# Optimization experiments

Measured on AMD Instinct MI355X. Metric: run time of the kernel, lower is better.

The kernel has to match this reference:

```python
import jax, jax.numpy as jnp
import numpy as np

GAMMA = 0.3      # LinearSpike surrogate slope (Bellec et al. 2018)
TIMESTEPS = 8
DROPOUT = 0.2

@jax.custom_vjp
def spike_fn(mem_thr):
    # forward: Heaviside spike; backward: piecewise-linear surrogate
    return (mem_thr > 0).astype(mem_thr.dtype)

def _spike_fwd(m):
    return (m > 0).astype(m.dtype), m

def _spike_bwd(m, g):
    return (GAMMA * jnp.maximum(1.0 - jnp.abs(m), 0.0) * g,)

spike_fn.defvjp(_spike_fwd, _spike_bwd)

def conv(x, w, stride=1, pad=1):
    return jax.lax.conv_general_dilated(
        x, w, (stride, stride), [(pad, pad), (pad, pad)],
        dimension_numbers=('NCHW', 'OIHW', 'NCHW'))

def avgpool2(x):
    B, C, H, W = x.shape
    return x.reshape(B, C, H // 2, 2, W // 2, 2).mean(axis=(3, 5))

def lif(mem, delta, leak, thr):
    mem = leak * mem + delta                  # leaky integrate
    mem_thr = mem / thr - 1.0                 # normalized membrane
    out = spike_fn(mem_thr)                   # binary spike
    mem = mem - thr * (mem_thr > 0).astype(mem.dtype)  # soft reset
    return mem, out

def setup_inputs() -> dict:
    key = jax.random.key(0)
    ks = jax.random.split(key, 24)
    B = 32
    def w(k, o, i, kh):
        std = float(np.sqrt(2.0 / (kh * kh * o)))  # matches _initialize_weights2
        return jax.random.normal(k, (o, i, kh, kh), jnp.float32) * std
    def mask(k, shape):
        keep = jax.random.bernoulli(k, 1.0 - DROPOUT, shape)
        return keep.astype(jnp.float32) / (1.0 - DROPOUT)
    return {
        'x': jax.random.normal(ks[0], (B, 3, 32, 32), jnp.float32),
        'w_pre0': w(ks[1], 64, 3, 3),
        'w_pre1': w(ks[2], 64, 64, 3),
        'w_pre2': w(ks[3], 64, 64, 3),
        'w1a': w(ks[4], 64, 64, 3),  'w1b': w(ks[5], 64, 64, 3),
        'w2a': w(ks[6], 128, 64, 3), 'w2b': w(ks[7], 128, 128, 3), 'w2i': w(ks[8], 128, 64, 1),
        'w3a': w(ks[9], 256, 128, 3), 'w3b': w(ks[10], 256, 256, 3), 'w3i': w(ks[11], 256, 128, 1),
        'w4a': w(ks[12], 512, 256, 3), 'w4b': w(ks[13], 512, 512, 3), 'w4i': w(ks[14], 512, 256, 1),
        'w_fc': jax.random.normal(ks[15], (10, 512 * 2 * 2), jnp.float32) * 0.01,
        'thr': jnp.ones((11,), jnp.float32),
        'leak': jnp.ones((11,), jnp.float32),
        'mask2': mask(ks[16], (B, 64, 32, 32)),
        'mask5': mask(ks[17], (B, 64, 32, 32)),
        'mask9': mask(ks[18], (B, 64, 16, 16)),
        'mask11': mask(ks[19], (B, 128, 8, 8)),
        'mask13': mask(ks[20], (B, 256, 4, 4)),
        'mask15': mask(ks[21], (B, 512, 2, 2)),
    }

def _forward(x, w_pre0, w_pre1, w_pre2, w1a, w1b, w2a, w2b, w2i,
             w3a, w3b, w3i, w4a, w4b, w4i, w_fc, thr, leak,
             mask2, mask5, mask9, mask11, mask13, mask15):
    B = x.shape[0]
    f32 = jnp.float32
    mems0 = (
        jnp.zeros((B, 64, 32, 32), f32), jnp.zeros((B, 64, 32, 32), f32),
        jnp.zeros((B, 64, 32, 32), f32),
        jnp.zeros((B, 64, 16, 16), f32), jnp.zeros((B, 64, 16, 16), f32),
        jnp.zeros((B, 128, 8, 8), f32), jnp.zeros((B, 128, 8, 8), f32),
        jnp.zeros((B, 256, 4, 4), f32), jnp.zeros((B, 256, 4, 4), f32),
        jnp.zeros((B, 512, 2, 2), f32), jnp.zeros((B, 512, 2, 2), f32),
        jnp.zeros((B, 10), f32),  # output accumulator mem
    )

    def step(carry, _):
        m0, m1, m2, m3, m4, m5, m6, m7, m8, m9, m10, mfc = carry
        # pre_process: (conv->spike->dropout) x2, conv->spike, avgpool2
        m0, o = lif(m0, conv(x, w_pre0), leak[0], thr[0]); o = o * mask2
        m1, o = lif(m1, conv(o, w_pre1), leak[1], thr[1]); o = o * mask5
        m2, o = lif(m2, conv(o, w_pre2), leak[2], thr[2])
        o = avgpool2(o)  # 32x32 -> 16x16
        # layer1 BasicBlock (stride 1, identity shortcut)
        inp = o
        m3, o = lif(m3, conv(inp, w1a), leak[3], thr[3]); o = o * mask9
        m4, o = lif(m4, conv(o, w1b) + inp, leak[4], thr[4])
        # layer2 BasicBlock (stride 2, 1x1 conv shortcut)
        inp = o
        m5, o = lif(m5, conv(inp, w2a, stride=2), leak[5], thr[5]); o = o * mask11
        m6, o = lif(m6, conv(o, w2b) + conv(inp, w2i, stride=2, pad=0), leak[6], thr[6])
        # layer3
        inp = o
        m7, o = lif(m7, conv(inp, w3a, stride=2), leak[7], thr[7]); o = o * mask13
        m8, o = lif(m8, conv(o, w3b) + conv(inp, w3i, stride=2, pad=0), leak[8], thr[8])
        # layer4
        inp = o
        m9, o = lif(m9, conv(inp, w4a, stride=2), leak[9], thr[9]); o = o * mask15
        m10, o = lif(m10, conv(o, w4b) + conv(inp, w4i, stride=2, pad=0), leak[10], thr[10])
        # output layer: pure accumulation of classifier current over timesteps
        mfc = mfc + o.reshape(B, -1) @ w_fc.T
        return (m0, m1, m2, m3, m4, m5, m6, m7, m8, m9, m10, mfc), None

    carry, _ = jax.lax.scan(step, mems0, None, length=TIMESTEPS)
    return carry[-1]  # [B, labels]

def reference(x, w_pre0, w_pre1, w_pre2, w1a, w1b, w2a, w2b, w2i,
              w3a, w3b, w3i, w4a, w4b, w4i, w_fc, thr, leak,
              mask2, mask5, mask9, mask11, mask13, mask15):
    return _forward(x, w_pre0, w_pre1, w_pre2, w1a, w1b, w2a, w2b, w2i,
                    w3a, w3b, w3i, w4a, w4b, w4i, w_fc, thr, leak,
                    mask2, mask5, mask9, mask11, mask13, mask15)
```

## Files before the change

### kernel.cpp

```cpp
#include <hip/hip_runtime.h>

#define BATCH 32

__device__ __forceinline__ float4 ld4(const float* p) { return *(const float4*)p; }

template<int H, int KS>
__global__ __launch_bounds__(256) void conv64_v2(
    const float* __restrict__ in, const float* __restrict__ w,
    float* __restrict__ pbuf)
{
    constexpr int W    = H;
    constexpr int QR   = W / 4;
    constexpr int ROWS = 64 / QR;
    constexpr int RS   = W + 4;
    constexpr int CCT  = 64 / KS;
    constexpr int CC   = (CCT < 8) ? CCT : 8;
    constexpr int NCH  = CCT / CC;
    constexpr int PLANE = (ROWS + 2) * RS;
    constexpr int NTOT = 32 * 64 * H * W;
    constexpr int LCNT = CC * (ROWS + 2) * (W + 2);
    static_assert(NCH == 1 || NCH == 2, "pipeline supports <=2 chunks");
    __shared__ float sIn[CC * PLANE];

    const int tid  = threadIdx.x;
    const int b    = blockIdx.x;
    const int rt   = blockIdx.y;
    const int zc   = blockIdx.z;
    const int cg   = zc & 1;
    const int ks   = zc >> 1;
    const int lane = tid & 63;
    const int g    = __builtin_amdgcn_readfirstlane(tid >> 6);
    const int octet = cg * 32 + g * 8;
    const int r    = lane / QR;
    const int wq   = lane % QR;
    const int ho   = rt * ROWS + r;
    const int row0 = rt * ROWS;

    float acc[8][4] = {};
    const size_t in_b = (size_t)b * 64 * H * W;

    auto stage_val = [&](int i, int c0, float& v) -> int {
        int c   = i / ((ROWS + 2) * (W + 2));
        int rr  = (i / (W + 2)) % (ROWS + 2);
        int col = i % (W + 2);
        int ih  = row0 + rr - 1;
        int iw  = col - 1;
        v = 0.f;
        if ((unsigned)ih < (unsigned)H && (unsigned)iw < (unsigned)W)
            v = in[in_b + (size_t)(c0 + c) * H * W + ih * W + iw];
        return c * PLANE + rr * RS + col;
    };

    auto compute_chunk = [&](int c0) {
        for (int c = 0; c < CC; ++c) {
            float rv[3][6];
            #pragma unroll
            for (int dr = 0; dr < 3; ++dr) {
                const float* p = &sIn[c * PLANE + (r + dr) * RS + wq * 4];
                float4 a  = ld4(p);
                float2 b2 = *(const float2*)(p + 4);
                rv[dr][0] = a.x;  rv[dr][1] = a.y; rv[dr][2] = a.z; rv[dr][3] = a.w;
                rv[dr][4] = b2.x; rv[dr][5] = b2.y;
            }
            const float* wc = w + ((size_t)octet * 64 + (c0 + c)) * 9;
            #pragma unroll
            for (int j = 0; j < 8; ++j) {
                const float* wk = wc + (size_t)j * 64 * 9;
                float w0 = wk[0], w1 = wk[1], w2 = wk[2];
                float w3 = wk[3], w4 = wk[4], w5 = wk[5];
                float w6 = wk[6], w7 = wk[7], w8 = wk[8];
                #pragma unroll
                for (int k = 0; k < 4; ++k) {
                    acc[j][k] = fmaf(rv[0][k + 0], w0, acc[j][k]);
                    acc[j][k] = fmaf(rv[0][k + 1], w1, acc[j][k]);
                    acc[j][k] = fmaf(rv[0][k + 2], w2, acc[j][k]);
                    acc[j][k] = fmaf(rv[1][k + 0], w3, acc[j][k]);
                    acc[j][k] = fmaf(rv[1][k + 1], w4, acc[j][k]);
                    acc[j][k] = fmaf(rv[1][k + 2], w5, acc[j][k]);
                    acc[j][k] = fmaf(rv[2][k + 0], w6, acc[j][k]);
                    acc[j][k] = fmaf(rv[2][k + 1], w7, acc[j][k]);
                    acc[j][k] = fmaf(rv[2][k + 2], w8, acc[j][k]);
                }
            }
        }
    };

    if constexpr (NCH == 1) {
        for (int i = tid; i < LCNT; i += 256) {
            float v; int o = stage_val(i, ks * CCT, v); sIn[o] = v;
        }
        __syncthreads();
        compute_chunk(ks * CCT);
    } else {
        for (int i = tid; i < LCNT; i += 256) {
            float v; int o = stage_val(i, ks * CCT, v); sIn[o] = v;
        }
        constexpr int PF = (LCNT + 255) / 256;
        float pf[PF]; int po[PF];
        #pragma unroll
        for (int k = 0; k < PF; ++k) {
            int i = tid + k * 256; pf[k] = 0.f; po[k] = -1;
            if (i < LCNT) po[k] = stage_val(i, ks * CCT + CC, pf[k]);
        }
        __syncthreads();
        compute_chunk(ks * CCT);
        __syncthreads();
        #pragma unroll
        for (int k = 0; k < PF; ++k) if (po[k] >= 0) sIn[po[k]] = pf[k];
        __syncthreads();
        compute_chunk(ks * CCT + CC);
    }

    #pragma unroll
    for (int j = 0; j < 8; ++j) {
        const size_t idx = ((size_t)(b * 64 + octet + j) * H + ho) * W + wq * 4;
        *(float4*)&pbuf[(size_t)ks * NTOT + idx] =
            make_float4(acc[j][0], acc[j][1], acc[j][2], acc[j][3]);
    }
}

template<int CI, int CO, int KS, int RT>
__global__ __launch_bounds__(256) void conv_mid(
    const float* __restrict__ in, const float* __restrict__ w,
    float* __restrict__ pbuf)
{
    constexpr int HIN = 16, HOUT = 8;
    constexpr int CC  = CI / KS;
    constexpr int NR  = (RT - 1) * 2 + 3;
    constexpr int BSTR = NR * HIN + 4;
    constexpr int CST  = 32 * BSTR;
    constexpr int NTOT = 32 * CO * HOUT * HOUT;
    __shared__ float sBuf[CC * CST];

    const int tid  = threadIdx.x;
    const int lane = tid & 63;
    const int b    = lane >> 1;
    const int ks   = blockIdx.x;
    const int co_u = __builtin_amdgcn_readfirstlane(blockIdx.y * 4 + (tid >> 6));
    const int r0   = blockIdx.z * RT;
    const int g0   = r0 * 2 - 1;

    for (int i = tid; i < CC * 32 * NR * 4; i += 256) {
        int q  = i % 4;
        int s  = (i / 4) % NR;
        int bb = (i / (4 * NR)) % 32;
        int c  = i / (4 * NR * 32);
        int gr = g0 + s;
        float4 v = make_float4(0.f, 0.f, 0.f, 0.f);
        if ((unsigned)gr < (unsigned)HIN)
            v = ld4(&in[(((size_t)bb * CI + ks * CC + c) * HIN + gr) * HIN + q * 4]);
        *(float4*)&sBuf[c * CST + bb * BSTR + s * HIN + q * 4] = v;
    }
    __syncthreads();

    float acc[RT * 8] = {};
    #pragma unroll
    for (int c = 0; c < CC; ++c) {
        const float* wk = w + ((size_t)co_u * CI + ks * CC + c) * 9;
        float wr[9];
        #pragma unroll
        for (int q = 0; q < 9; ++q) wr[q] = wk[q];
        float pl[NR * HIN];
        #pragma unroll
        for (int k = 0; k < NR * 4; ++k) {
            float4 v = ld4(&sBuf[c * CST + b * BSTR + k * 4]);
            pl[k * 4 + 0] = v.x; pl[k * 4 + 1] = v.y;
            pl[k * 4 + 2] = v.z; pl[k * 4 + 3] = v.w;
        }
        #pragma unroll
        for (int j = 0; j < RT; ++j) {
            #pragma unroll
            for (int ow = 0; ow < 8; ++ow) {
                #pragma unroll
                for (int kh = 0; kh < 3; ++kh) {
                    const int s = 2 * j + kh;
                    #pragma unroll
                    for (int kw = 0; kw < 3; ++kw) {
                        const int iw = 2 * ow - 1 + kw;
                        if (iw < 0 || iw >= HIN) continue;
                        acc[j * 8 + ow] = fmaf(pl[s * HIN + iw], wr[kh * 3 + kw],
                                               acc[j * 8 + ow]);
                    }
                }
            }
        }
    }

    if ((lane & 1) == 0) {
        #pragma unroll
        for (int j = 0; j < RT; ++j) {
            const size_t idx = ((size_t)(b * CO + co_u) * HOUT + r0 + j) * HOUT;
            *(float4*)&pbuf[(size_t)ks * NTOT + idx] =
                make_float4(acc[j * 8 + 0], acc[j * 8 + 1], acc[j * 8 + 2], acc[j * 8 + 3]);
            *(float4*)&pbuf[(size_t)ks * NTOT + idx + 4] =
                make_float4(acc[j * 8 + 4], acc[j * 8 + 5], acc[j * 8 + 6], acc[j * 8 + 7]);
        }
    }
}

template<int KS>
__global__ __launch_bounds__(256) void conv_l2b(
    const float* __restrict__ in,
    const float* __restrict__ w,
    const float* __restrict__ sc_in,
    const float* __restrict__ sc_w,
    float* __restrict__ pbuf)
{
    constexpr int CI = 128, CO = 128, SC_CI = 64;
    constexpr int CC  = CI / KS;
    constexpr int SCC = SC_CI / KS;
    constexpr int BSTR = 52, CST = 32 * BSTR;
    constexpr int BSTRs = 36, CSTs = 32 * BSTRs;
    constexpr int NTOT = 32 * CO * 64;
    __shared__ float sBuf[CC * CST];

    const int tid  = threadIdx.x;
    const int lane = tid & 63;
    const int b    = lane >> 1;
    const int co_u = __builtin_amdgcn_readfirstlane(blockIdx.y * 4 + (tid >> 6));
    const int ks   = blockIdx.x;
    const int r0   = blockIdx.z * 4;

    for (int i = tid; i < CC * 32 * 12; i += 256) {
        int f4  = i % 2;
        int row = (i / 2) % 6;
        int bb  = (i / 12) % 32;
        int c   = i / 384;
        int gr  = r0 - 1 + row;
        float4 v = make_float4(0.f, 0.f, 0.f, 0.f);
        if ((unsigned)gr < 8u)
            v = ld4(&in[(((size_t)bb * CI + ks * CC + c) * 8 + gr) * 8 + f4 * 4]);
        *(float4*)&sBuf[c * CST + bb * BSTR + row * 8 + f4 * 4] = v;
    }
    __syncthreads();

    float acc[32] = {};
    #pragma unroll
    for (int c = 0; c < CC; ++c) {
        const float* wk = w + ((size_t)co_u * CI + ks * CC + c) * 9;
        float wr[9];
        #pragma unroll
        for (int q = 0; q < 9; ++q) wr[q] = wk[q];
        float pl[48];
        #pragma unroll
        for (int k = 0; k < 12; ++k) {
            float4 v = ld4(&sBuf[c * CST + b * BSTR + k * 4]);
            pl[k * 4 + 0] = v.x; pl[k * 4 + 1] = v.y;
            pl[k * 4 + 2] = v.z; pl[k * 4 + 3] = v.w;
        }
        #pragma unroll
        for (int oh = 0; oh < 4; ++oh) {
            #pragma unroll
            for (int ow = 0; ow < 8; ++ow) {
                #pragma unroll
                for (int kh = 0; kh < 3; ++kh) {
                    #pragma unroll
                    for (int kw = 0; kw < 3; ++kw) {
                        const int iw = ow - 1 + kw;
                        if (iw < 0 || iw >= 8) continue;
                        acc[oh * 8 + ow] = fmaf(pl[(oh + kh) * 8 + iw],
                                                wr[kh * 3 + kw], acc[oh * 8 + ow]);
                    }
                }
            }
        }
    }
    __syncthreads();

    for (int i = tid; i < SCC * 32 * 16; i += 256) {
        int q   = i % 4;
        int row = (i / 4) % 4;
        int bb  = (i / 16) % 32;
        int c   = i / 512;
        float4 v = ld4(&sc_in[
            (((size_t)bb * SC_CI + ks * SCC + c) * 16 + 2 * (r0 + row)) * 16 + q * 4]);
        sBuf[c * CSTs + bb * BSTRs + row * 8 + q * 2 + 0] = v.x;
        sBuf[c * CSTs + bb * BSTRs + row * 8 + q * 2 + 1] = v.z;
    }
    __syncthreads();

    #pragma unroll
    for (int c = 0; c < SCC; ++c) {
        float sw = sc_w[(size_t)co_u * SC_CI + ks * SCC + c];
        #pragma unroll
        for (int p4 = 0; p4 < 8; ++p4) {
            float4 v = ld4(&sBuf[c * CSTs + b * BSTRs + p4 * 4]);
            acc[p4 * 4 + 0] = fmaf(v.x, sw, acc[p4 * 4 + 0]);
            acc[p4 * 4 + 1] = fmaf(v.y, sw, acc[p4 * 4 + 1]);
            acc[p4 * 4 + 2] = fmaf(v.z, sw, acc[p4 * 4 + 2]);
            acc[p4 * 4 + 3] = fmaf(v.w, sw, acc[p4 * 4 + 3]);
        }
    }

    if ((lane & 1) == 0) {
        #pragma unroll
        for (int oh = 0; oh < 4; ++oh) {
            const size_t idx = ((size_t)(b * CO + co_u) * 8 + r0 + oh) * 8;
            *(float4*)&pbuf[(size_t)ks * NTOT + idx]     =
                make_float4(acc[oh * 8 + 0], acc[oh * 8 + 1], acc[oh * 8 + 2], acc[oh * 8 + 3]);
            *(float4*)&pbuf[(size_t)ks * NTOT + idx + 4] =
                make_float4(acc[oh * 8 + 4], acc[oh * 8 + 5], acc[oh * 8 + 6], acc[oh * 8 + 7]);
        }
    }
}

template<int CI, int HIN, int STRIDE, int CO, int SC_CI, int SC_HIN,
         int KS, int COB>
__global__ __launch_bounds__(COB * 64) void conv_ks(
    const float* __restrict__ in, const float* __restrict__ w,
    const float* __restrict__ sc_in, const float* __restrict__ sc_w,
    float* __restrict__ pbuf)
{
    constexpr int NT   = COB * 64;
    constexpr int HOUT = (STRIDE == 2) ? HIN / 2 : HIN;
    constexpr int P    = HOUT * HOUT;
    constexpr int NPIX = HIN * HIN;
    constexpr int CC   = CI / KS;
    constexpr int SCC  = (SC_CI > 0) ? SC_CI / KS : 0;
    constexpr int BSTR = NPIX + (((NPIX / 4) % 2 == 0) ? 4 : 0);
    constexpr int CST  = 32 * BSTR;
    constexpr int BSTRs = P + (((P / 4) % 2 == 0) ? 4 : 0);
    constexpr int CSTs  = 32 * BSTRs;
    static_assert(CI % KS == 0, "ks split");
    static_assert(NPIX % 4 == 0 && P % 4 == 0, "vector widths");

    __shared__ float sIn[CC * CST];
    __shared__ float sSc[(SCC > 0) ? SCC * CSTs : 1];

    const int tid  = threadIdx.x;
    const int lane = tid & 63;
    const int b    = lane >> 1;
    const int ks   = blockIdx.x;
    const int co_u = __builtin_amdgcn_readfirstlane(blockIdx.y * COB + (tid >> 6));
    const int cb   = ks * CC;

    constexpr int NF4 = CC * 32 * (NPIX / 4);
    for (int i = tid; i < NF4; i += NT) {
        int k4 = i % (NPIX / 4);
        int c  = (i / (NPIX / 4)) % CC;
        int bb = i / ((NPIX / 4) * CC);
        float4 v = ld4(&in[((size_t)bb * CI + cb + c) * NPIX + k4 * 4]);
        *(float4*)&sIn[c * CST + bb * BSTR + k4 * 4] = v;
    }
    if constexpr (SCC > 0) {
        constexpr int NH  = HOUT / 2;
        constexpr int NSC = SCC * 32 * HOUT * NH;
        for (int i = tid; i < NSC; i += NT) {
            int hc = i % NH;
            int r  = (i / NH) % HOUT;
            int c  = (i / (NH * HOUT)) % SCC;
            int bb = i / (NH * HOUT * SCC);
            float4 v = ld4(&sc_in[
                ((size_t)(bb * SC_CI + ks * SCC + c) * SC_HIN + 2 * r) * SC_HIN
                + hc * 4]);
            sSc[c * CSTs + bb * BSTRs + r * HOUT + hc * 2 + 0] = v.x;
            sSc[c * CSTs + bb * BSTRs + r * HOUT + hc * 2 + 1] = v.z;
        }
    }
    __syncthreads();

    float acc[P] = {};

    const float* wbase = w + ((size_t)co_u * CI + cb) * 9;
    #pragma unroll 4
    for (int j = 0; j < CC; ++j) {
        float wr[9];
        #pragma unroll
        for (int q = 0; q < 9; ++q) wr[q] = wbase[j * 9 + q];
        float plane[NPIX];
        #pragma unroll
        for (int r4 = 0; r4 < NPIX / 4; ++r4) {
            float4 v = ld4(&sIn[j * CST + b * BSTR + r4 * 4]);
            plane[r4 * 4 + 0] = v.x; plane[r4 * 4 + 1] = v.y;
            plane[r4 * 4 + 2] = v.z; plane[r4 * 4 + 3] = v.w;
        }
        #pragma unroll
        for (int ho = 0; ho < HOUT; ++ho) {
            #pragma unroll
            for (int wo = 0; wo < HOUT; ++wo) {
                #pragma unroll
                for (int kh = 0; kh < 3; ++kh) {
                    const int ih = ho * STRIDE - 1 + kh;
                    if (ih < 0 || ih >= HIN) continue;
                    #pragma unroll
                    for (int kw = 0; kw < 3; ++kw) {
                        const int iw = wo * STRIDE - 1 + kw;
                        if (iw < 0 || iw >= HIN) continue;
                        acc[ho * HOUT + wo] =
                            fmaf(plane[ih * HIN + iw], wr[kh * 3 + kw],
                                 acc[ho * HOUT + wo]);
                    }
                }
            }
        }
    }

    if constexpr (SCC > 0) {
        const float* swb = sc_w + (size_t)co_u * SC_CI + ks * SCC;
        #pragma unroll 4
        for (int j = 0; j < SCC; ++j) {
            float sw = swb[j];
            #pragma unroll
            for (int p4 = 0; p4 < P / 4; ++p4) {
                float4 v = ld4(&sSc[j * CSTs + b * BSTRs + p4 * 4]);
                acc[p4 * 4 + 0] = fmaf(v.x, sw, acc[p4 * 4 + 0]);
                acc[p4 * 4 + 1] = fmaf(v.y, sw, acc[p4 * 4 + 1]);
                acc[p4 * 4 + 2] = fmaf(v.z, sw, acc[p4 * 4 + 2]);
                acc[p4 * 4 + 3] = fmaf(v.w, sw, acc[p4 * 4 + 3]);
            }
        }
    }

    if ((lane & 1) == 0) {
        float* pp = pbuf + (((size_t)ks * 32 + b) * CO + co_u) * P;
        #pragma unroll
        for (int p4 = 0; p4 < P / 4; ++p4)
            *(float4*)&pp[p4 * 4] = make_float4(acc[p4 * 4], acc[p4 * 4 + 1],
                                                acc[p4 * 4 + 2], acc[p4 * 4 + 3]);
    }
}

template<int CO, int P, int KS>
__global__ __launch_bounds__(256) void reduce_lif(
    const float* __restrict__ pbuf,
    const float* __restrict__ res,
    float* __restrict__ mem,
    const float* __restrict__ thr_a, const float* __restrict__ leak_a, int layer,
    const float* __restrict__ mask, float* __restrict__ out,
    float* __restrict__ accum)
{
    constexpr int TOT4 = 32 * CO * P / 4;
    const int i4 = blockIdx.x * 256 + threadIdx.x;
    if (i4 >= TOT4) return;
    const float4* pb4 = (const float4*)pbuf;
    float4 s = pb4[i4];
    #pragma unroll 4
    for (int ks = 1; ks < KS; ++ks) {
        float4 v = pb4[(size_t)ks * TOT4 + i4];
        s.x += v.x; s.y += v.y; s.z += v.z; s.w += v.w;
    }
    const size_t idx = (size_t)i4 * 4;
    if (res) {
        float4 r4 = ld4(&res[idx]);
        s.x += r4.x; s.y += r4.y; s.z += r4.z; s.w += r4.w;
    }
    const float thr  = thr_a[layer];
    const float leak = leak_a[layer];
    float4 m4 = ld4(&mem[idx]);
    float4 k4 = mask ? ld4(&mask[idx]) : make_float4(1.f, 1.f, 1.f, 1.f);
    float4 mo, oo;
    float m0 = fmaf(leak, m4.x, s.x); float s0 = (m0 / thr - 1.0f > 0.f) ? 1.f : 0.f;
    mo.x = m0 - thr * s0; oo.x = s0 * k4.x;
    float m1 = fmaf(leak, m4.y, s.y); float s1 = (m1 / thr - 1.0f > 0.f) ? 1.f : 0.f;
    mo.y = m1 - thr * s1; oo.y = s1 * k4.y;
    float m2 = fmaf(leak, m4.z, s.z); float s2 = (m2 / thr - 1.0f > 0.f) ? 1.f : 0.f;
    mo.z = m2 - thr * s2; oo.z = s2 * k4.z;
    float m3 = fmaf(leak, m4.w, s.w); float s3 = (m3 / thr - 1.0f > 0.f) ? 1.f : 0.f;
    mo.w = m3 - thr * s3; oo.w = s3 * k4.w;
    *(float4*)&mem[idx] = mo;
    *(float4*)&out[idx] = oo;
    if (accum) {
        float4 a4 = ld4(&accum[idx]);
        a4.x += oo.x; a4.y += oo.y; a4.z += oo.z; a4.w += oo.w;
        *(float4*)&accum[idx] = a4;
    }
}

template<int KS>
__global__ __launch_bounds__(256) void reduce_lif_pool(
    const float* __restrict__ pbuf, float* __restrict__ mem,
    const float* __restrict__ thr_a, const float* __restrict__ leak_a, int layer,
    float* __restrict__ pool_out)
{
    constexpr int TOT = 32 * 64 * 32 * 32;
    const int i = blockIdx.x * 256 + threadIdx.x;
    const int q  = i % 8;
    const int rp = (i / 8) % 16;
    const int c  = (i / 128) % 64;
    const int b  = i / 8192;
    const size_t idx0 = (((size_t)(b * 64 + c) * 32) + 2 * rp) * 32 + 4 * q;
    const size_t idx1 = idx0 + 32;

    float4 s0 = ld4(&pbuf[idx0]);
    float4 s1 = ld4(&pbuf[idx1]);
    #pragma unroll 4
    for (int ks = 1; ks < KS; ++ks) {
        float4 v0 = ld4(&pbuf[(size_t)ks * TOT + idx0]);
        float4 v1 = ld4(&pbuf[(size_t)ks * TOT + idx1]);
        s0.x += v0.x; s0.y += v0.y; s0.z += v0.z; s0.w += v0.w;
        s1.x += v1.x; s1.y += v1.y; s1.z += v1.z; s1.w += v1.w;
    }
    const float thr  = thr_a[layer];
    const float leak = leak_a[layer];
    float4 m0 = ld4(&mem[idx0]), m1 = ld4(&mem[idx1]);
    float4 n0, n1, o0, o1;
    {
        float m = fmaf(leak, m0.x, s0.x); float sp = (m / thr - 1.0f > 0.f) ? 1.f : 0.f;
        n0.x = m - thr * sp; o0.x = sp;
        m = fmaf(leak, m0.y, s0.y); sp = (m / thr - 1.0f > 0.f) ? 1.f : 0.f;
        n0.y = m - thr * sp; o0.y = sp;
        m = fmaf(leak, m0.z, s0.z); sp = (m / thr - 1.0f > 0.f) ? 1.f : 0.f;
        n0.z = m - thr * sp; o0.z = sp;
        m = fmaf(leak, m0.w, s0.w); sp = (m / thr - 1.0f > 0.f) ? 1.f : 0.f;
        n0.w = m - thr * sp; o0.w = sp;
        m = fmaf(leak, m1.x, s1.x); sp = (m / thr - 1.0f > 0.f) ? 1.f : 0.f;
        n1.x = m - thr * sp; o1.x = sp;
        m = fmaf(leak, m1.y, s1.y); sp = (m / thr - 1.0f > 0.f) ? 1.f : 0.f;
        n1.y = m - thr * sp; o1.y = sp;
        m = fmaf(leak, m1.z, s1.z); sp = (m / thr - 1.0f > 0.f) ? 1.f : 0.f;
        n1.z = m - thr * sp; o1.z = sp;
        m = fmaf(leak, m1.w, s1.w); sp = (m / thr - 1.0f > 0.f) ? 1.f : 0.f;
        n1.w = m - thr * sp; o1.w = sp;
    }
    *(float4*)&mem[idx0] = n0;
    *(float4*)&mem[idx1] = n1;
    float2 pv;
    pv.x = (o0.x + o0.y + o1.x + o1.y) * 0.25f;
    pv.y = (o0.z + o0.w + o1.z + o1.w) * 0.25f;
    *(float2*)&pool_out[(((size_t)(b * 64 + c) * 16) + rp) * 16 + 2 * q] = pv;
}

__global__ __launch_bounds__(256) void conv_raw_kernel(
    const float* __restrict__ in, const float* __restrict__ w,
    float* __restrict__ out,
    int Ci, int Co, int Hin, int Win, int total)
{
    int idx = blockIdx.x * blockDim.x + threadIdx.x;
    if (idx >= total) return;
    int wo = idx % Win;
    int t  = idx / Win;
    int ho = t % Hin; t /= Hin;
    int co = t % Co;
    int b  = t / Co;
    int ih0 = ho - 1, iw0 = wo - 1;
    const float* wp = w + (size_t)co * Ci * 9;
    const float* ip = in + (size_t)b * Ci * Hin * Win;
    bool hv0 = (unsigned)(ih0)     < (unsigned)Hin;
    bool hv1 = (unsigned)(ih0 + 1) < (unsigned)Hin;
    bool hv2 = (unsigned)(ih0 + 2) < (unsigned)Hin;
    bool wv0 = (unsigned)(iw0)     < (unsigned)Win;
    bool wv1 = (unsigned)(iw0 + 1) < (unsigned)Win;
    bool wv2 = (unsigned)(iw0 + 2) < (unsigned)Win;
    float acc = 0.f;
    int plane = Hin * Win;
    for (int ci = 0; ci < Ci; ++ci) {
        const float* irow = ip + ci * plane;
        const float* wk   = wp + ci * 9;
        if (hv0) {
            const float* r = irow + ih0 * Win;
            if (wv0) acc = fmaf(r[iw0],     wk[0], acc);
            if (wv1) acc = fmaf(r[iw0 + 1], wk[1], acc);
            if (wv2) acc = fmaf(r[iw0 + 2], wk[2], acc);
        }
        if (hv1) {
            const float* r = irow + (ih0 + 1) * Win;
            if (wv0) acc = fmaf(r[iw0],     wk[3], acc);
            if (wv1) acc = fmaf(r[iw0 + 1], wk[4], acc);
            if (wv2) acc = fmaf(r[iw0 + 2], wk[5], acc);
        }
        if (hv2) {
            const float* r = irow + (ih0 + 2) * Win;
            if (wv0) acc = fmaf(r[iw0],     wk[6], acc);
            if (wv1) acc = fmaf(r[iw0 + 1], wk[7], acc);
            if (wv2) acc = fmaf(r[iw0 + 2], wk[8], acc);
        }
    }
    out[idx] = acc;
}

__global__ __launch_bounds__(256) void lif0_kernel(
    const float4* __restrict__ delta, float4* __restrict__ mem,
    const float* __restrict__ thr_a, const float* __restrict__ leak_a,
    const float4* __restrict__ mask, float4* __restrict__ out, int total4)
{
    int i = blockIdx.x * blockDim.x + threadIdx.x;
    if (i >= total4) return;
    float thr = thr_a[0], leak = leak_a[0];
    float4 d = delta[i], m4 = mem[i], k4 = mask[i], mo, oo;
    float m0 = fmaf(leak, m4.x, d.x); float s0 = (m0 / thr - 1.0f > 0.f) ? 1.f : 0.f;
    mo.x = m0 - thr * s0; oo.x = s0 * k4.x;
    float m1 = fmaf(leak, m4.y, d.y); float s1 = (m1 / thr - 1.0f > 0.f) ? 1.f : 0.f;
    mo.y = m1 - thr * s1; oo.y = s1 * k4.y;
    float m2 = fmaf(leak, m4.z, d.z); float s2 = (m2 / thr - 1.0f > 0.f) ? 1.f : 0.f;
    mo.z = m2 - thr * s2; oo.z = s2 * k4.z;
    float m3 = fmaf(leak, m4.w, d.w); float s3 = (m3 / thr - 1.0f > 0.f) ? 1.f : 0.f;
    mo.w = m3 - thr * s3; oo.w = s3 * k4.w;
    mem[i] = mo; out[i] = oo;
}

__global__ __launch_bounds__(64) void fc_kernel(
    const float* __restrict__ s, const float* __restrict__ wfc,
    float* __restrict__ out)
{
    int bk = blockIdx.x;
    int b = bk / 10, k = bk % 10;
    const float* sp = s   + (size_t)b * 2048;
    const float* wp = wfc + (size_t)k * 2048;
    float acc = 0.f;
    for (int j = threadIdx.x; j < 2048; j += 64)
        acc = fmaf(sp[j], wp[j], acc);
    #pragma unroll
    for (int off = 32; off; off >>= 1)
        acc += __shfl_down(acc, off, 64);
    if (threadIdx.x == 0) out[b * 10 + k] = acc;
}

extern "C" void kernel_launch(void* const* d_in, const int* in_sizes, int n_in,
                              void* d_out, int out_size, void* d_ws, size_t ws_size,
                              hipStream_t stream) {
    const float* x      = (const float*)d_in[0];
    const float* w_pre0 = (const float*)d_in[1];
    const float* w_pre1 = (const float*)d_in[2];
    const float* w_pre2 = (const float*)d_in[3];
    const float* w1a    = (const float*)d_in[4];
    const float* w1b    = (const float*)d_in[5];
    const float* w2a    = (const float*)d_in[6];
    const float* w2b    = (const float*)d_in[7];
    const float* w2i    = (const float*)d_in[8];
    const float* w3a    = (const float*)d_in[9];
    const float* w3b    = (const float*)d_in[10];
    const float* w3i    = (const float*)d_in[11];
    const float* w4a    = (const float*)d_in[12];
    const float* w4b    = (const float*)d_in[13];
    const float* w4i    = (const float*)d_in[14];
    const float* w_fc   = (const float*)d_in[15];
    const float* thr    = (const float*)d_in[16];
    const float* leak   = (const float*)d_in[17];
    const float* mask2  = (const float*)d_in[18];
    const float* mask5  = (const float*)d_in[19];
    const float* mask9  = (const float*)d_in[20];
    const float* mask11 = (const float*)d_in[21];
    const float* mask13 = (const float*)d_in[22];
    const float* mask15 = (const float*)d_in[23];

    float* ws = (float*)d_ws;
    size_t off = 0;
    auto alloc = [&](size_t n) { float* p = ws + off; off += n; return p; };
    float* m0  = alloc(2097152);
    float* m1  = alloc(2097152);
    float* m2  = alloc(2097152);
    float* m3  = alloc(524288);
    float* m4  = alloc(524288);
    float* m5  = alloc(262144);
    float* m6  = alloc(262144);
    float* m7  = alloc(131072);
    float* m8  = alloc(131072);
    float* m9  = alloc(65536);
    float* m10 = alloc(65536);
    float* ssum = alloc(65536);
    size_t zero_floats = off;
    float* delta0  = alloc(2097152);
    float* s32_a   = alloc(2097152);
    float* s32_b   = alloc(2097152);
    float* s16_inp = alloc(524288);
    float* s16_a   = alloc(524288);
    float* s16_b   = alloc(524288);
    float* s8_a    = alloc(262144);
    float* s8_b    = alloc(262144);
    float* s4_a    = alloc(131072);
    float* s4_b    = alloc(131072);
    float* s2_a    = alloc(65536);
    float* s2_b    = alloc(65536);
    float* pbuf    = alloc(16777216);
    (void)ws_size; (void)in_sizes; (void)n_in; (void)out_size;

    hipMemsetAsync(d_ws, 0, zero_floats * sizeof(float), stream);

    auto grid = [](int total) { return dim3((total + 255) / 256); };

    {
        int total = BATCH * 64 * 32 * 32;
        conv_raw_kernel<<<grid(total), 256, 0, stream>>>(
            x, w_pre0, delta0, 3, 64, 32, 32, total);
    }

    for (int t = 0; t < 8; ++t) {
        int n32 = BATCH * 64 * 32 * 32;
        lif0_kernel<<<grid(n32 / 4), 256, 0, stream>>>(
            (const float4*)delta0, (float4*)m0, thr, leak,
            (const float4*)mask2, (float4*)s32_a, n32 / 4);
        conv64_v2<32, 4><<<dim3(BATCH, 4, 8), 256, 0, stream>>>(s32_a, w_pre1, pbuf);
        reduce_lif<64, 1024, 4><<<dim3(2048), 256, 0, stream>>>(
            pbuf, nullptr, m1, thr, leak, 1, mask5, s32_b, nullptr);
        conv64_v2<32, 4><<<dim3(BATCH, 4, 8), 256, 0, stream>>>(s32_b, w_pre2, pbuf);
        reduce_lif_pool<4><<<dim3(1024), 256, 0, stream>>>(
            pbuf, m2, thr, leak, 2, s16_inp);
        conv64_v2<16, 8><<<dim3(BATCH, 1, 16), 256, 0, stream>>>(s16_inp, w1a, pbuf);
        reduce_lif<64, 256, 8><<<dim3(512), 256, 0, stream>>>(
            pbuf, nullptr, m3, thr, leak, 3, mask9, s16_a, nullptr);
        conv64_v2<16, 8><<<dim3(BATCH, 1, 16), 256, 0, stream>>>(s16_a, w1b, pbuf);
        reduce_lif<64, 256, 8><<<dim3(512), 256, 0, stream>>>(
            pbuf, s16_inp, m4, thr, leak, 4, nullptr, s16_b, nullptr);

        conv_mid<64, 128, 32, 2><<<dim3(32, 32, 4), 256, 0, stream>>>(
            s16_b, w2a, pbuf);
        reduce_lif<128, 64, 32><<<dim3(256), 256, 0, stream>>>(
            pbuf, nullptr, m5, thr, leak, 5, mask11, s8_a, nullptr);
        conv_l2b<32><<<dim3(32, 32, 2), 256, 0, stream>>>(
            s8_a, w2b, s16_b, w2i, pbuf);
        reduce_lif<128, 64, 32><<<dim3(256), 256, 0, stream>>>(
            pbuf, nullptr, m6, thr, leak, 6, nullptr, s8_b, nullptr);
        conv_ks<128, 8, 2, 256, 0, 0, 32, 4><<<dim3(32, 64), 256, 0, stream>>>(
            s8_b, w3a, nullptr, nullptr, pbuf);
        reduce_lif<256, 16, 32><<<dim3(128), 256, 0, stream>>>(
            pbuf, nullptr, m7, thr, leak, 7, mask13, s4_a, nullptr);
        conv_ks<256, 4, 1, 256, 128, 8, 16, 4><<<dim3(16, 64), 256, 0, stream>>>(
            s4_a, w3b, s8_b, w3i, pbuf);
        reduce_lif<256, 16, 16><<<dim3(128), 256, 0, stream>>>(
            pbuf, nullptr, m8, thr, leak, 8, nullptr, s4_b, nullptr);
        conv_ks<256, 4, 2, 512, 0, 0, 16, 4><<<dim3(16, 128), 256, 0, stream>>>(
            s4_b, w4a, nullptr, nullptr, pbuf);
        reduce_lif<512, 4, 16><<<dim3(64), 256, 0, stream>>>(
            pbuf, nullptr, m9, thr, leak, 9, mask15, s2_a, nullptr);
        conv_ks<512, 2, 1, 512, 256, 4, 16, 4><<<dim3(16, 128), 256, 0, stream>>>(
            s2_a, w4b, s4_b, w4i, pbuf);
        reduce_lif<512, 4, 16><<<dim3(64), 256, 0, stream>>>(
            pbuf, nullptr, m10, thr, leak, 10, nullptr, s2_b, ssum);
    }

    fc_kernel<<<dim3(320), dim3(64), 0, stream>>>(ssum, w_fc, (float*)d_out);
}
```

Before: 2.845 ms.

## Fuse next-step layer0 LIF into final reduce, retune unroll and l2b split

The layer-0 LIF launch is merged into the last reduce kernel of the previous timestep, using extra blocks, which drops one launch per step. Layer 2b's conv now uses a 16-way channel split instead of 32, so the following reduce reads fewer partial sums. The conv channel loop is unrolled by 2 instead of fully, which lowers register pressure but may cost some instruction-level parallelism. The fused kernel mixes a tiny reduce with a large elementwise pass.

```diff
diff --git a/kernel.cpp b/kernel.cpp
--- a/kernel.cpp
+++ b/kernel.cpp
@@ -235,7 +235,7 @@
     __syncthreads();
 
     float acc[32] = {};
-    #pragma unroll
+    #pragma unroll 2
     for (int c = 0; c < CC; ++c) {
         const float* wk = w + ((size_t)co_u * CI + ks * CC + c) * 9;
         float wr[9];
@@ -420,32 +420,11 @@
     }
 }
 
-template<int CO, int P, int KS>
-__global__ __launch_bounds__(256) void reduce_lif(
-    const float* __restrict__ pbuf,
-    const float* __restrict__ res,
-    float* __restrict__ mem,
-    const float* __restrict__ thr_a, const float* __restrict__ leak_a, int layer,
-    const float* __restrict__ mask, float* __restrict__ out,
-    float* __restrict__ accum)
-{
-    constexpr int TOT4 = 32 * CO * P / 4;
-    const int i4 = blockIdx.x * 256 + threadIdx.x;
-    if (i4 >= TOT4) return;
-    const float4* pb4 = (const float4*)pbuf;
-    float4 s = pb4[i4];
-    #pragma unroll 4
-    for (int ks = 1; ks < KS; ++ks) {
-        float4 v = pb4[(size_t)ks * TOT4 + i4];
-        s.x += v.x; s.y += v.y; s.z += v.z; s.w += v.w;
-    }
-    const size_t idx = (size_t)i4 * 4;
-    if (res) {
-        float4 r4 = ld4(&res[idx]);
-        s.x += r4.x; s.y += r4.y; s.z += r4.z; s.w += r4.w;
-    }
-    const float thr  = thr_a[layer];
-    const float leak = leak_a[layer];
+__device__ __forceinline__ void lif_store4(
+    float4 s, float* __restrict__ mem, const float* __restrict__ mask,
+    float* __restrict__ out, float* __restrict__ accum,
+    size_t idx, float thr, float leak)
+{
     float4 m4 = ld4(&mem[idx]);
     float4 k4 = mask ? ld4(&mask[idx]) : make_float4(1.f, 1.f, 1.f, 1.f);
     float4 mo, oo;
@@ -464,6 +443,33 @@
         a4.x += oo.x; a4.y += oo.y; a4.z += oo.z; a4.w += oo.w;
         *(float4*)&accum[idx] = a4;
     }
+}
+
+template<int CO, int P, int KS>
+__global__ __launch_bounds__(256) void reduce_lif(
+    const float* __restrict__ pbuf,
+    const float* __restrict__ res,
+    float* __restrict__ mem,
+    const float* __restrict__ thr_a, const float* __restrict__ leak_a, int layer,
+    const float* __restrict__ mask, float* __restrict__ out,
+    float* __restrict__ accum)
+{
+    constexpr int TOT4 = 32 * CO * P / 4;
+    const int i4 = blockIdx.x * 256 + threadIdx.x;
+    if (i4 >= TOT4) return;
+    const float4* pb4 = (const float4*)pbuf;
+    float4 s = pb4[i4];
+    #pragma unroll 4
+    for (int ks = 1; ks < KS; ++ks) {
+        float4 v = pb4[(size_t)ks * TOT4 + i4];
+        s.x += v.x; s.y += v.y; s.z += v.z; s.w += v.w;
+    }
+    const size_t idx = (size_t)i4 * 4;
+    if (res) {
+        float4 r4 = ld4(&res[idx]);
+        s.x += r4.x; s.y += r4.y; s.z += r4.z; s.w += r4.w;
+    }
+    lif_store4(s, mem, mask, out, accum, idx, thr_a[layer], leak_a[layer]);
 }
 
 template<int KS>
@@ -518,6 +524,43 @@
     pv.x = (o0.x + o0.y + o1.x + o1.y) * 0.25f;
     pv.y = (o0.z + o0.w + o1.z + o1.w) * 0.25f;
     *(float2*)&pool_out[(((size_t)(b * 64 + c) * 16) + rp) * 16 + 2 * q] = pv;
+}
+
+template<int KS>
+__global__ __launch_bounds__(256) void reduce_l4b_lif0(
+    const float* __restrict__ pbuf, float* __restrict__ mem10,
+    const float* __restrict__ thr_a, const float* __restrict__ leak_a,
+    float* __restrict__ out_s2b, float* __restrict__ ssum,
+    const float4* __restrict__ delta, float4* __restrict__ mem0,
+    const float4* __restrict__ mask, float4* __restrict__ s32a)
+{
+    if (blockIdx.x < 64) {
+        constexpr int TOT4 = 32 * 512;
+        const int i4 = blockIdx.x * 256 + threadIdx.x;
+        if (i4 >= TOT4) return;
+        const float4* pb4 = (const float4*)pbuf;
+        float4 s = pb4[i4];
+        #pragma unroll 4
+        for (int ks = 1; ks < KS; ++ks) {
+            float4 v = pb4[(size_t)ks * TOT4 + i4];
+            s.x += v.x; s.y += v.y; s.z += v.z; s.w += v.w;
+        }
+        lif_store4(s, mem10, nullptr, out_s2b, ssum,
+                   (size_t)i4 * 4, thr_a[10], leak_a[10]);
+    } else {
+        const int i = (blockIdx.x - 64) * 256 + threadIdx.x;
+        float thr = thr_a[0], leak = leak_a[0];
+        float4 d = delta[i], m4 = mem0[i], k4 = mask[i], mo, oo;
+        float m0 = fmaf(leak, m4.x, d.x); float s0 = (m0 / thr - 1.0f > 0.f) ? 1.f : 0.f;
+        mo.x = m0 - thr * s0; oo.x = s0 * k4.x;
+        float m1 = fmaf(leak, m4.y, d.y); float s1 = (m1 / thr - 1.0f > 0.f) ? 1.f : 0.f;
+        mo.y = m1 - thr * s1; oo.y = s1 * k4.y;
+        float m2 = fmaf(leak, m4.z, d.z); float s2 = (m2 / thr - 1.0f > 0.f) ? 1.f : 0.f;
+        mo.z = m2 - thr * s2; oo.z = s2 * k4.z;
+        float m3 = fmaf(leak, m4.w, d.w); float s3 = (m3 / thr - 1.0f > 0.f) ? 1.f : 0.f;
+        mo.w = m3 - thr * s3; oo.w = s3 * k4.w;
+        mem0[i] = mo; s32a[i] = oo;
+    }
 }
 
 __global__ __launch_bounds__(256) void conv_raw_kernel(
@@ -674,11 +717,12 @@
             x, w_pre0, delta0, 3, 64, 32, 32, total);
     }
 
+    int n32 = BATCH * 64 * 32 * 32;
+    lif0_kernel<<<grid(n32 / 4), 256, 0, stream>>>(
+        (const float4*)delta0, (float4*)m0, thr, leak,
+        (const float4*)mask2, (float4*)s32_a, n32 / 4);
+
     for (int t = 0; t < 8; ++t) {
-        int n32 = BATCH * 64 * 32 * 32;
-        lif0_kernel<<<grid(n32 / 4), 256, 0, stream>>>(
-            (const float4*)delta0, (float4*)m0, thr, leak,
-            (const float4*)mask2, (float4*)s32_a, n32 / 4);
         conv64_v2<32, 4><<<dim3(BATCH, 4, 8), 256, 0, stream>>>(s32_a, w_pre1, pbuf);
         reduce_lif<64, 1024, 4><<<dim3(2048), 256, 0, stream>>>(
             pbuf, nullptr, m1, thr, leak, 1, mask5, s32_b, nullptr);
@@ -696,9 +740,9 @@
             s16_b, w2a, pbuf);
         reduce_lif<128, 64, 32><<<dim3(256), 256, 0, stream>>>(
             pbuf, nullptr, m5, thr, leak, 5, mask11, s8_a, nullptr);
-        conv_l2b<32><<<dim3(32, 32, 2), 256, 0, stream>>>(
+        conv_l2b<16><<<dim3(16, 32, 2), 256, 0, stream>>>(
             s8_a, w2b, s16_b, w2i, pbuf);
-        reduce_lif<128, 64, 32><<<dim3(256), 256, 0, stream>>>(
+        reduce_lif<128, 64, 16><<<dim3(256), 256, 0, stream>>>(
             pbuf, nullptr, m6, thr, leak, 6, nullptr, s8_b, nullptr);
         conv_ks<128, 8, 2, 256, 0, 0, 32, 4><<<dim3(32, 64), 256, 0, stream>>>(
             s8_b, w3a, nullptr, nullptr, pbuf);
@@ -714,8 +758,15 @@
             pbuf, nullptr, m9, thr, leak, 9, mask15, s2_a, nullptr);
         conv_ks<512, 2, 1, 512, 256, 4, 16, 4><<<dim3(16, 128), 256, 0, stream>>>(
             s2_a, w4b, s4_b, w4i, pbuf);
-        reduce_lif<512, 4, 16><<<dim3(64), 256, 0, stream>>>(
-            pbuf, nullptr, m10, thr, leak, 10, nullptr, s2_b, ssum);
+        if (t < 7) {
+            reduce_l4b_lif0<16><<<dim3(64 + 2048), 256, 0, stream>>>(
+                pbuf, m10, thr, leak, s2_b, ssum,
+                (const float4*)delta0, (float4*)m0, (const float4*)mask2,
+                (float4*)s32_a);
+        } else {
+            reduce_lif<512, 4, 16><<<dim3(64), 256, 0, stream>>>(
+                pbuf, nullptr, m10, thr, leak, 10, nullptr, s2_b, ssum);
+        }
     }
 
     fc_kernel<<<dim3(320), dim3(64), 0, stream>>>(ssum, w_fc, (float*)d_out);
```

Result: faster. 2.755 ms (-3.1%).
